# Kernel optimization log

Hardware: AMD Instinct MI355X
Metric: run time of the kernel (lower is better)

The kernel has to match this reference:

```python
import math
import jax, jax.numpy as jnp
import numpy as np

HEADS = 8
LOG_APPROX_VAR = math.log(0.01)  # self.var = 0.01, non-trainable


def clustering(x, approx_log_var, mu, log_var, log_prior):
    """Faithful port of DisentangledAttention.clustering (mi_estimation=False).
    x: [B,H,L,D]; approx_log_var: [B,H,L]; mu/log_var: [H,C,D]; log_prior: [H,C].
    Returns (cluster_probs [B,H,L,C], kl_loss [B,1,1], div_loss [B])."""
    B, H, L, D = x.shape
    xe = x[:, :, :, None, :]                      # [B,H,L,1,D]
    mue = mu[:, None, :, :]                       # [H,1,C,D]
    alv = approx_log_var[:, :, :, None, None]     # [B,H,L,1,1]
    avar = jnp.exp(alv)
    lv = log_var[:, None, :, :]                   # [H,1,C,D]
    var = jnp.exp(lv)
    logp = jax.nn.log_softmax(log_prior, axis=-1)  # [H,C]

    mse = (xe - mue) ** 2 / var                   # [B,H,L,C,D]
    log_pdf = -0.5 * mse.sum(-1) - D * math.pi - 0.5 * lv.sum(-1)  # [B,H,L,C]
    log_pdf = log_pdf + logp[:, None, :]
    log_probs = jax.nn.log_softmax(log_pdf, axis=-1)
    probs = jnp.exp(log_probs)                    # [B,H,L,C]

    logp_b = logp[None, :, None, :]               # broadcast prior log-probs
    prior = jnp.exp(logp_b)
    # F.kl_div(log_probs, prior) = prior * (log(prior) - log_probs)
    kl = (prior * (logp_b - log_probs)).sum(-1).mean(axis=(1, 2))            # [B]
    kl = kl + 0.5 * (probs * (mse + avar / var + lv).sum(-1)).sum(-1).mean(axis=(1, 2))
    kl = kl - 0.5 * jnp.mean(((1.0 + alv).sum(-1)) * D, axis=(1, 2, 3))
    kl_loss = kl.reshape(-1, 1, 1)

    eyeL = jnp.eye(L, dtype=x.dtype)
    div = jnp.einsum('bhqc,bhkc->bhqk', probs, probs)   # [B,H,L,L]
    div = (div - eyeL) ** 2
    wmask = eyeL * 1.25 + (1.0 - eyeL) * 0.75
    div_loss = (div * wmask).mean(axis=(1, 2, 3))       # [B]
    return probs, kl_loss, div_loss


def setup_inputs() -> dict:
    k = jax.random.key(0)
    ks = jax.random.split(k, 10)
    B, L, D, H, C = 4, 1024, 512, HEADS, 8
    Dk = D // H
    lin_std = 1.0 / math.sqrt(2.0 * D)  # xavier_normal gain=1/sqrt(2)
    return {
        'query': jax.random.normal(ks[0], (B, L, D), jnp.float32),
        'key': jax.random.normal(ks[1], (B, L, D), jnp.float32),
        'value': jax.random.normal(ks[2], (B, L, D), jnp.float32),
        'padding_mask': jnp.zeros((B, 1, L), jnp.float32),
        'Wq': jax.random.normal(ks[3], (D, D), jnp.float32) * lin_std,
        'bq': jnp.zeros((D,), jnp.float32),
        'Wk': jax.random.normal(ks[4], (D, D), jnp.float32) * lin_std,
        'bk': jnp.zeros((D,), jnp.float32),
        'Wv': jax.random.normal(ks[5], (D, D), jnp.float32) * lin_std,
        'bv': jnp.zeros((D,), jnp.float32),
        'Wo': jax.random.normal(ks[6], (D, D), jnp.float32) * lin_std,
        'bo': jnp.zeros((D,), jnp.float32),
        'tok_mu': jax.random.normal(ks[7], (H, C, Dk), jnp.float32) * 0.1,
        'tok_log_var': jnp.zeros((H, C, Dk), jnp.float32),
        'tok_log_prior': jnp.full((H, C), math.log(1.0 / C), jnp.float32),
    }


def reference(query, key, value, padding_mask, Wq, bq, Wk, bk, Wv, bv, Wo, bo,
              tok_mu, tok_log_var, tok_log_prior):
    B, L, D = query.shape
    H = HEADS
    Dk = D // H

    # GMM clustering on raw (unprojected) per-head query/key, eval mode (no reparam noise)
    qh = query.reshape(B, L, H, Dk).transpose(0, 2, 1, 3)  # [B,H,L,Dk]
    kh = key.reshape(B, L, H, Dk).transpose(0, 2, 1, 3)
    alv = jnp.full((B, H, L), LOG_APPROX_VAR, dtype=query.dtype)
    probs_q, kl_q, div_q = clustering(qh, alv, tok_mu, tok_log_var, tok_log_prior)
    probs_k, kl_k, div_k = clustering(kh, alv, tok_mu, tok_log_var, tok_log_prior)

    # Disentangled mask: tokens sharing clusters attend (mask==1 means blocked)
    sim = jnp.einsum('bhqc,bhkc->bhqk', probs_q, probs_k)   # [B,H,L,L]
    cmask = jnp.clip(1.0 - sim + padding_mask[:, :, None, :], 0.0, 1.0)

    # Projections + scaled softmax attention (per softmax_attention/full_attention)
    q = (query @ Wq.T + bq).reshape(B, L, H, Dk).transpose(0, 2, 1, 3) / math.sqrt(Dk)
    kk = (key @ Wk.T + bk).reshape(B, L, H, Dk).transpose(0, 2, 1, 3)
    v = (value @ Wv.T + bv).reshape(B, L, H, Dk).transpose(0, 2, 1, 3)
    scores = jnp.einsum('bhqd,bhkd->bhqk', q, kk) + jax.lax.stop_gradient(cmask) * (-10000.0)
    attn = jax.nn.softmax(scores, axis=-1) * (1.0 - cmask)
    out = jnp.einsum('bhqk,bhkd->bhqd', attn, v).transpose(0, 2, 1, 3).reshape(B, L, D)
    out = out @ Wo.T + bo

    kl_loss = kl_q + kl_k                      # [B,1,1]
    div_loss = (div_q + div_k).reshape(-1, 1, 1)  # [B,1,1]
    return out, kl_loss, div_loss
```

## Files before the change

### kernel.cpp

```cpp
#include <hip/hip_runtime.h>
#include <hip/hip_bf16.h>
#include <math.h>

#define NB 4
#define NL 1024
#define ND 512
#define NH 8
#define NC 8
#define NDK 64

static constexpr float KL3_CONST = 115.36544595161891f;

typedef __bf16 bf16x8 __attribute__((ext_vector_type(8)));
typedef float  f32x4v __attribute__((ext_vector_type(4)));
typedef unsigned short u16x4 __attribute__((ext_vector_type(4)));
typedef unsigned short u16x8 __attribute__((ext_vector_type(8)));

__device__ __forceinline__ unsigned short bf16u(float f) {
    return __builtin_bit_cast(unsigned short, (__bf16)f);
}

struct GemmArgs {
    const void* A; const float* W; const float* bias; void* out;
    float scale; int abf; int obf; int brow; int ostr; int vmap;
};

__device__ __forceinline__ void gemm_body(const GemmArgs& g, unsigned char* smem)
{
    unsigned short* As = (unsigned short*)smem;
    unsigned short* Ws = (unsigned short*)(smem + 5120);
    const int tid = threadIdx.x;
    int n0, m0;
    if (g.vmap) {
        const int linear = blockIdx.y * 4 + blockIdx.x;
        n0 = (linear & 31) * 128;
        m0 = (linear >> 5) * 64;
    } else {
        n0 = blockIdx.x * 128;
        m0 = blockIdx.y * 64;
    }

    const int w = tid >> 6, lane = tid & 63;
    const int r16 = lane & 15, quad = lane >> 4;
    const int arow = tid >> 2, akc = tid & 3;
    const int wrow = tid >> 1, wkc = tid & 1;

    f32x4v acc[8];
#pragma unroll
    for (int n = 0; n < 8; ++n) acc[n] = (f32x4v){0.f, 0.f, 0.f, 0.f};

    auto ldA = [&](int k0) -> u16x8 {
        if (g.abf) {
            return *(const u16x8*)((const unsigned short*)g.A + (size_t)(m0 + arow) * 512 + k0 + akc * 8);
        }
        const float* ap = (const float*)g.A + (size_t)(m0 + arow) * 512 + k0 + akc * 8;
        const float4 a0 = *(const float4*)ap, a1 = *(const float4*)(ap + 4);
        return (u16x8){ bf16u(a0.x), bf16u(a0.y), bf16u(a0.z), bf16u(a0.w),
                        bf16u(a1.x), bf16u(a1.y), bf16u(a1.z), bf16u(a1.w) };
    };
    auto ldW = [&](int k0, u16x8* dst) {
        const float* wp = (const float*)g.W + (size_t)(n0 + wrow) * 512 + k0 + wkc * 16;
        const float4 w0 = *(const float4*)wp,       w1 = *(const float4*)(wp + 4);
        const float4 w2 = *(const float4*)(wp + 8), w3 = *(const float4*)(wp + 12);
        dst[0] = (u16x8){ bf16u(w0.x), bf16u(w0.y), bf16u(w0.z), bf16u(w0.w),
                          bf16u(w1.x), bf16u(w1.y), bf16u(w1.z), bf16u(w1.w) };
        dst[1] = (u16x8){ bf16u(w2.x), bf16u(w2.y), bf16u(w2.z), bf16u(w2.w),
                          bf16u(w3.x), bf16u(w3.y), bf16u(w3.z), bf16u(w3.w) };
    };
    auto store_stage = [&](const u16x8& sa, const u16x8* sw) {
        *(u16x8*)(As + arow * 40 + akc * 8) = sa;
        *(u16x8*)(Ws + wrow * 40 + wkc * 16) = sw[0];
        *(u16x8*)(Ws + wrow * 40 + wkc * 16 + 8) = sw[1];
    };
    auto mfma_half = [&]() {
        bf16x8 af = *(const bf16x8*)(As + (w * 16 + r16) * 40 + quad * 8);
#pragma unroll
        for (int ni = 0; ni < 8; ++ni) {
            bf16x8 bfr = *(const bf16x8*)(Ws + (ni * 16 + r16) * 40 + quad * 8);
            acc[ni] = __builtin_amdgcn_mfma_f32_16x16x32_bf16(af, bfr, acc[ni], 0, 0, 0);
        }
    };

    u16x8 sa0 = ldA(0),  sw0[2]; ldW(0, sw0);
    u16x8 sa1 = ldA(32), sw1[2]; ldW(32, sw1);

    for (int k0 = 0; k0 < 512; k0 += 64) {
        __syncthreads();
        store_stage(sa0, sw0);
        __syncthreads();
        if (k0 + 64 < 512) { sa0 = ldA(k0 + 64); ldW(k0 + 64, sw0); }
        mfma_half();

        __syncthreads();
        store_stage(sa1, sw1);
        __syncthreads();
        if (k0 + 96 < 512) { sa1 = ldA(k0 + 96); ldW(k0 + 96, sw1); }
        mfma_half();
    }

#pragma unroll
    for (int ni = 0; ni < 8; ++ni) {
        const int col = n0 + ni * 16 + r16;
        const float bcol = g.brow ? 0.f : g.bias[col];
#pragma unroll
        for (int i = 0; i < 4; ++i) {
            const int row = m0 + w * 16 + quad * 4 + i;
            const float bv = g.brow ? g.bias[row] : bcol;
            const float v = (acc[ni][i] + bv) * g.scale;
            if (g.obf) ((unsigned short*)g.out)[(size_t)row * g.ostr + col] = bf16u(v);
            else       ((float*)g.out)[(size_t)row * g.ostr + col] = v;
        }
    }
}

__device__ __forceinline__ void cluster_body(
    const float* __restrict__ query, const float* __restrict__ key,
    const float* __restrict__ tok_mu, const float* __restrict__ tok_log_var,
    const float* __restrict__ tok_log_prior,
    float* __restrict__ probs_q, float* __restrict__ probs_k,
    float* __restrict__ klp, float* __restrict__ divp, float* __restrict__ Gp,
    int linear, unsigned char* smem)
{
    float* mu_s    = (float*)smem;
    float* iv_s    = (float*)(smem + 2048);
    float* Pl      = (float*)(smem + 4096);
    float* Gpart   = (float*)(smem + 13312);
    float* red_s   = (float*)(smem + 14336);
    float* lvsum_s = (float*)(smem + 14368);
    float* alpha_s = (float*)(smem + 14400);
    float* logp_s  = (float*)(smem + 14432);
    float* prior_s = (float*)(smem + 14464);

    const int tid  = threadIdx.x;
    const int side = linear >> 7;
    const int rem  = linear & 127;
    const int bh   = rem >> 2, chunk = rem & 3;
    const int b    = bh >> 3, h = bh & 7;
    const int blocklin = side * 128 + bh * 4 + chunk;
    const float* src = side ? key : query;
    float* probs_out = side ? probs_k : probs_q;

    for (int i = tid; i < 512; i += 256) {
        mu_s[i] = tok_mu[h * 512 + i];
        float lv = tok_log_var[h * 512 + i];
        iv_s[i] = __expf(-lv);
    }
    if (tid < 8) {
        float ls = 0.f, al = 0.f;
        for (int d = 0; d < 64; ++d) {
            float lv = tok_log_var[(h * 8 + tid) * 64 + d];
            ls += lv;
            al += 0.01f * __expf(-lv) + lv;
        }
        lvsum_s[tid] = ls; alpha_s[tid] = al;
    }
    if (tid == 0) {
        float lp[8]; float mx = -1e30f;
        for (int c = 0; c < 8; ++c) { lp[c] = tok_log_prior[h * 8 + c]; mx = fmaxf(mx, lp[c]); }
        float se = 0.f;
        for (int c = 0; c < 8; ++c) se += __expf(lp[c] - mx);
        float lse = mx + __logf(se);
        for (int c = 0; c < 8; ++c) { logp_s[c] = lp[c] - lse; prior_s[c] = __expf(lp[c] - lse); }
    }
    __syncthreads();

    const int l = chunk * 256 + tid;
    const float4* xp = (const float4*)(src + ((size_t)(b * NL + l)) * ND + h * NDK);
    float4 xr[16];
#pragma unroll
    for (int i = 0; i < 16; ++i) xr[i] = xp[i];

    float ms[8];
#pragma unroll
    for (int c = 0; c < 8; ++c) {
        const float4* mc = (const float4*)(mu_s + c * 64);
        const float4* ic = (const float4*)(iv_s + c * 64);
        float s = 0.f;
#pragma unroll
        for (int i = 0; i < 16; ++i) {
            float4 m4 = mc[i], v4 = ic[i], x4 = xr[i];
            float dx = x4.x - m4.x; s = fmaf(dx * dx, v4.x, s);
            float dy = x4.y - m4.y; s = fmaf(dy * dy, v4.y, s);
            float dz = x4.z - m4.z; s = fmaf(dz * dz, v4.z, s);
            float dw = x4.w - m4.w; s = fmaf(dw * dw, v4.w, s);
        }
        ms[c] = s;
    }

    float lpdf[8]; float mx = -1e30f;
#pragma unroll
    for (int c = 0; c < 8; ++c) {
        lpdf[c] = -0.5f * (ms[c] + lvsum_s[c]) + logp_s[c];
        mx = fmaxf(mx, lpdf[c]);
    }
    float e[8]; float se = 0.f;
#pragma unroll
    for (int c = 0; c < 8; ++c) { e[c] = __expf(lpdf[c] - mx); se += e[c]; }
    float lse = __logf(se);
    float inv = 1.f / se;
    float p[8]; float kl1 = 0.f, kl2 = 0.f, sqq = 0.f;
#pragma unroll
    for (int c = 0; c < 8; ++c) {
        p[c] = e[c] * inv;
        float logprob = lpdf[c] - mx - lse;
        kl1 += prior_s[c] * (logp_s[c] - logprob);
        kl2 += p[c] * (ms[c] + alpha_s[c]);
        sqq = fmaf(p[c], p[c], sqq);
    }

    float* po = probs_out + ((size_t)((b * NH + h) * NL + l)) * NC;
    ((float4*)po)[0] = make_float4(p[0], p[1], p[2], p[3]);
    ((float4*)po)[1] = make_float4(p[4], p[5], p[6], p[7]);
#pragma unroll
    for (int c = 0; c < 8; ++c) Pl[tid * 9 + c] = p[c];

    float dterm = 1.25f * (sqq - 1.f) * (sqq - 1.f) - 0.75f * sqq * sqq;
    float klv = kl1 + 0.5f * kl2;
    __syncthreads();

    {
        int qt = tid >> 6, pos = tid & 63, c1 = pos >> 3, c2 = pos & 7;
        float g = 0.f;
        for (int i = 0; i < 64; ++i) {
            int ll = qt * 64 + i;
            g = fmaf(Pl[ll * 9 + c1], Pl[ll * 9 + c2], g);
        }
        Gpart[qt * 64 + pos] = g;
    }

#pragma unroll
    for (int o = 32; o > 0; o >>= 1) {
        klv   += __shfl_down(klv, o);
        dterm += __shfl_down(dterm, o);
    }
    if ((tid & 63) == 0) { red_s[tid >> 6] = klv; red_s[4 + (tid >> 6)] = dterm; }
    __syncthreads();
    if (tid == 0) {
        klp[blocklin]  = red_s[0] + red_s[1] + red_s[2] + red_s[3];
        divp[blocklin] = red_s[4] + red_s[5] + red_s[6] + red_s[7];
    }
    if (tid < 64)
        Gp[(size_t)blocklin * 64 + tid] =
            Gpart[tid] + Gpart[64 + tid] + Gpart[128 + tid] + Gpart[192 + tid];
}

__global__ __launch_bounds__(256) void fused_front(
    GemmArgs g0, GemmArgs g1, GemmArgs g2,
    const float* query, const float* key,
    const float* tok_mu, const float* tok_log_var, const float* tok_log_prior,
    float* probs_q, float* probs_k,
    float* klp, float* divp, float* Gp)
{
    __shared__ alignas(16) unsigned char smem[15488];
    if (blockIdx.z == 3) {
        const int linear = blockIdx.y * 4 + blockIdx.x;
        cluster_body(query, key, tok_mu, tok_log_var, tok_log_prior,
                     probs_q, probs_k, klp, divp, Gp, linear, smem);
        return;
    }
    GemmArgs g = (blockIdx.z == 0) ? g0 : ((blockIdx.z == 1) ? g1 : g2);
    gemm_body(g, smem);
}

#define APAD 72

__global__ __launch_bounds__(128) void attn_mfma3s_kernel(
    const unsigned short* __restrict__ qp16, const unsigned short* __restrict__ kp16,
    const unsigned short* __restrict__ vtp16,
    const float* __restrict__ probs_q, const float* __restrict__ probs_k,
    const float* __restrict__ padding_mask,
    float* __restrict__ pO, float* __restrict__ pML)
{
    const int tid = threadIdx.x, lane = tid & 63, w = tid >> 6;
    const int r16 = lane & 15, quad = lane >> 4;
    const int b = blockIdx.z >> 1, s = blockIdx.z & 1;
    const int h = blockIdx.y;
    const int qt = blockIdx.x;
    const int qbase = qt * 32;
    const int sb = ((b * 8 + h) << 5) | qt;

    __shared__ alignas(16) unsigned short Ks[64 * APAD];
    __shared__ alignas(16) unsigned short Vt[64 * APAD];
    __shared__ alignas(16) unsigned short Ps[2][16 * APAD];
    __shared__ float pk_s[8 * 65];
    __shared__ float pm_s[64];

    bf16x8 qa[2];
    {
        const unsigned short* qrow = qp16 + ((size_t)(b * NL + qbase + w * 16 + r16)) * ND + h * NDK;
        qa[0] = *(const bf16x8*)(qrow + quad * 8);
        qa[1] = *(const bf16x8*)(qrow + 32 + quad * 8);
    }
    float pq[4][8];
#pragma unroll
    for (int i = 0; i < 4; ++i) {
        const float* pr = probs_q + ((size_t)((b * NH + h) * NL + qbase + w * 16 + quad * 4 + i)) * NC;
        float4 a = ((const float4*)pr)[0], c = ((const float4*)pr)[1];
        pq[i][0] = a.x; pq[i][1] = a.y; pq[i][2] = a.z; pq[i][3] = a.w;
        pq[i][4] = c.x; pq[i][5] = c.y; pq[i][6] = c.z; pq[i][7] = c.w;
    }

    f32x4v oacc[4];
#pragma unroll
    for (int n = 0; n < 4; ++n) oacc[n] = (f32x4v){0.f, 0.f, 0.f, 0.f};
    float m_i[4] = {-1e30f, -1e30f, -1e30f, -1e30f};
    float l_i[4] = {0.f, 0.f, 0.f, 0.f};

    for (int kt = 0; kt < 8; ++kt) {
        const int key0 = s * 512 + kt * 64;
        __syncthreads();

#pragma unroll
        for (int i = 0; i < 4; ++i) {
            const int c = i * 128 + tid;
            const int row = c >> 3, c8 = c & 7;
            u16x8 kv = *(const u16x8*)(kp16 + ((size_t)(b * NL + key0 + row)) * ND + h * NDK + c8 * 8);
            *(u16x8*)(Ks + row * APAD + c8 * 8) = kv;
            u16x8 vv = *(const u16x8*)(vtp16 + ((size_t)(h * 64 + row)) * (NB * NL) + b * NL + key0 + c8 * 8);
            *(u16x8*)(Vt + row * APAD + c8 * 8) = vv;
        }
        {
            const int key = tid >> 1, half = tid & 1;
            float4 p = *(const float4*)(probs_k + ((size_t)((b * NH + h) * NL + key0 + key)) * NC + half * 4);
            pk_s[(half * 4 + 0) * 65 + key] = p.x;
            pk_s[(half * 4 + 1) * 65 + key] = p.y;
            pk_s[(half * 4 + 2) * 65 + key] = p.z;
            pk_s[(half * 4 + 3) * 65 + key] = p.w;
        }
        if (tid < 64) pm_s[tid] = padding_mask[b * NL + key0 + tid];
        __syncthreads();

        f32x4v sacc[4];
#pragma unroll
        for (int t = 0; t < 4; ++t) {
            sacc[t] = (f32x4v){0.f, 0.f, 0.f, 0.f};
            bf16x8 kb0 = *(const bf16x8*)(Ks + (t * 16 + r16) * APAD + quad * 8);
            bf16x8 kb1 = *(const bf16x8*)(Ks + (t * 16 + r16) * APAD + 32 + quad * 8);
            sacc[t] = __builtin_amdgcn_mfma_f32_16x16x32_bf16(qa[0], kb0, sacc[t], 0, 0, 0);
            sacc[t] = __builtin_amdgcn_mfma_f32_16x16x32_bf16(qa[1], kb1, sacc[t], 0, 0, 0);
        }

        float sc[4][4], wgt[4][4];
#pragma unroll
        for (int t = 0; t < 4; ++t) {
            const int keyl = t * 16 + r16;
            float pkc[8];
#pragma unroll
            for (int c = 0; c < 8; ++c) pkc[c] = pk_s[c * 65 + keyl];
            const float pmv = pm_s[keyl];
#pragma unroll
            for (int i = 0; i < 4; ++i) {
                float sim = 0.f;
#pragma unroll
                for (int c = 0; c < 8; ++c) sim = fmaf(pq[i][c], pkc[c], sim);
                float cm = 1.f - sim + pmv;
                cm = fminf(fmaxf(cm, 0.f), 1.f);
                sc[t][i] = sacc[t][i] - 10000.f * cm;
                wgt[t][i] = 1.f - cm;
            }
        }

        float mx[4];
#pragma unroll
        for (int i = 0; i < 4; ++i)
            mx[i] = fmaxf(fmaxf(sc[0][i], sc[1][i]), fmaxf(sc[2][i], sc[3][i]));
#pragma unroll
        for (int o = 1; o < 16; o <<= 1) {
#pragma unroll
            for (int i = 0; i < 4; ++i) mx[i] = fmaxf(mx[i], __shfl_xor(mx[i], o));
        }
        float rr[4];
#pragma unroll
        for (int i = 0; i < 4; ++i) {
            const float mnew = fmaxf(m_i[i], mx[i]);
            rr[i] = __expf(m_i[i] - mnew);
            m_i[i] = mnew;
            l_i[i] *= rr[i];
        }
#pragma unroll
        for (int n = 0; n < 4; ++n) {
            oacc[n][0] *= rr[0]; oacc[n][1] *= rr[1];
            oacc[n][2] *= rr[2]; oacc[n][3] *= rr[3];
        }
        float lad[4] = {0.f, 0.f, 0.f, 0.f};
#pragma unroll
        for (int t = 0; t < 4; ++t) {
#pragma unroll
            for (int i = 0; i < 4; ++i) {
                const float p = __expf(sc[t][i] - m_i[i]);
                lad[i] += p;
                Ps[w][(quad * 4 + i) * APAD + t * 16 + r16] = bf16u(p * wgt[t][i]);
            }
        }
#pragma unroll
        for (int o = 1; o < 16; o <<= 1) {
#pragma unroll
            for (int i = 0; i < 4; ++i) lad[i] += __shfl_xor(lad[i], o);
        }
#pragma unroll
        for (int i = 0; i < 4; ++i) l_i[i] += lad[i];

        bf16x8 pa0 = *(const bf16x8*)(Ps[w] + r16 * APAD + quad * 8);
        bf16x8 pa1 = *(const bf16x8*)(Ps[w] + r16 * APAD + 32 + quad * 8);
#pragma unroll
        for (int n = 0; n < 4; ++n) {
            bf16x8 vb0 = *(const bf16x8*)(Vt + (n * 16 + r16) * APAD + quad * 8);
            bf16x8 vb1 = *(const bf16x8*)(Vt + (n * 16 + r16) * APAD + 32 + quad * 8);
            oacc[n] = __builtin_amdgcn_mfma_f32_16x16x32_bf16(pa0, vb0, oacc[n], 0, 0, 0);
            oacc[n] = __builtin_amdgcn_mfma_f32_16x16x32_bf16(pa1, vb1, oacc[n], 0, 0, 0);
        }
    }

    float* po = pO + ((size_t)sb * 2 + s) * 2048;
#pragma unroll
    for (int i = 0; i < 4; ++i) {
        const int row = w * 16 + quad * 4 + i;
#pragma unroll
        for (int n = 0; n < 4; ++n)
            po[row * 64 + n * 16 + r16] = oacc[n][i];
    }
    if (r16 == 0) {
        float* pml = pML + ((size_t)sb * 2 + s) * 64;
#pragma unroll
        for (int i = 0; i < 4; ++i) {
            const int row = w * 16 + quad * 4 + i;
            pml[row * 2]     = m_i[i];
            pml[row * 2 + 1] = l_i[i];
        }
    }
}

__device__ __forceinline__ void finalize_body(
    const float* __restrict__ klp, const float* __restrict__ divp,
    const float* __restrict__ Gp, float* __restrict__ out_tail)
{
    const int tid = threadIdx.x, b = tid >> 6, lane = tid & 63;
    float gsum = 0.f;
#pragma unroll
    for (int s = 0; s < 2; ++s)
#pragma unroll
        for (int h = 0; h < 8; ++h) {
            const int base = s * 128 + (b * 8 + h) * 4;
            float Ge = 0.f;
#pragma unroll
            for (int x = 0; x < 4; ++x) Ge += Gp[(size_t)(base + x) * 64 + lane];
            gsum = fmaf(Ge, Ge, gsum);
        }
    const int s = lane >> 5, rem = lane & 31, h = rem >> 2, x = rem & 3;
    const int idx = s * 128 + (b * 8 + h) * 4 + x;
    float klv = klp[idx];
    float dvv = divp[idx];
#pragma unroll
    for (int o = 32; o > 0; o >>= 1) {
        gsum += __shfl_down(gsum, o);
        klv  += __shfl_down(klv, o);
        dvv  += __shfl_down(dvv, o);
    }
    if (lane == 0) {
        out_tail[b]     = klv * (1.0f / 8192.0f) + 2.0f * KL3_CONST;
        out_tail[4 + b] = (dvv + 0.75f * gsum) * (1.0f / 8388608.0f);
    }
}

__global__ __launch_bounds__(256) void merge_fin_kernel(
    const float* __restrict__ pO, const float* __restrict__ pML,
    unsigned short* __restrict__ ao16,
    const float* __restrict__ klp, const float* __restrict__ divp,
    const float* __restrict__ Gp, float* __restrict__ out_tail)
{
    if (blockIdx.x == 1024) { finalize_body(klp, divp, Gp, out_tail); return; }
    const int gid = blockIdx.x * 256 + threadIdx.x;
    const int sb = gid >> 8, rem = gid & 255;
    const int row = rem >> 3, d0 = (rem & 7) * 8;

    const float2 ml0 = *(const float2*)(pML + ((size_t)sb * 2 + 0) * 64 + row * 2);
    const float2 ml1 = *(const float2*)(pML + ((size_t)sb * 2 + 1) * 64 + row * 2);
    const float M = fmaxf(ml0.x, ml1.x);
    const float e0 = __expf(ml0.x - M), e1 = __expf(ml1.x - M);
    const float inv = 1.f / fmaf(ml0.y, e0, ml1.y * e1);
    const float f0 = e0 * inv, f1 = e1 * inv;

    const float* p0 = pO + ((size_t)sb * 2 + 0) * 2048 + row * 64 + d0;
    const float* p1 = pO + ((size_t)sb * 2 + 1) * 2048 + row * 64 + d0;
    const int qt = sb & 31, bh = sb >> 5, h = bh & 7, b = bh >> 3;
    unsigned short* orow = ao16 + ((size_t)(b * NL + qt * 32 + row)) * ND + h * NDK + d0;

    const float4 a0 = *(const float4*)p0,       a1 = *(const float4*)(p0 + 4);
    const float4 c0 = *(const float4*)p1,       c1 = *(const float4*)(p1 + 4);
    u16x8 ov = { bf16u(a0.x * f0 + c0.x * f1), bf16u(a0.y * f0 + c0.y * f1),
                 bf16u(a0.z * f0 + c0.z * f1), bf16u(a0.w * f0 + c0.w * f1),
                 bf16u(a1.x * f0 + c1.x * f1), bf16u(a1.y * f0 + c1.y * f1),
                 bf16u(a1.z * f0 + c1.z * f1), bf16u(a1.w * f0 + c1.w * f1) };
    *(u16x8*)orow = ov;
}

__global__ __launch_bounds__(256) void gemm_single(GemmArgs g)
{
    __shared__ alignas(16) unsigned char smem[15488];
    gemm_body(g, smem);
}

extern "C" void kernel_launch(void* const* d_in, const int* in_sizes, int n_in,
                              void* d_out, int out_size, void* d_ws, size_t ws_size,
                              hipStream_t stream)
{
    const float* query        = (const float*)d_in[0];
    const float* key          = (const float*)d_in[1];
    const float* value        = (const float*)d_in[2];
    const float* padding_mask = (const float*)d_in[3];
    const float* Wq = (const float*)d_in[4];
    const float* bq = (const float*)d_in[5];
    const float* Wk = (const float*)d_in[6];
    const float* bk = (const float*)d_in[7];
    const float* Wv = (const float*)d_in[8];
    const float* bv = (const float*)d_in[9];
    const float* Wo = (const float*)d_in[10];
    const float* bo = (const float*)d_in[11];
    const float* tok_mu        = (const float*)d_in[12];
    const float* tok_log_var   = (const float*)d_in[13];
    const float* tok_log_prior = (const float*)d_in[14];

    float* ws = (float*)d_ws;
    const size_t FS = 1048576;
    unsigned short* qp16  = (unsigned short*)ws;
    unsigned short* kp16  = (unsigned short*)(ws + FS);
    unsigned short* vtp16 = (unsigned short*)(ws + 2 * FS);
    unsigned short* ao16  = (unsigned short*)(ws + 3 * FS);
    float* probs_q = ws + 4 * FS;
    float* probs_k = probs_q + (size_t)NB * NH * NL * NC;
    float* pO      = probs_k + (size_t)NB * NH * NL * NC;
    float* pML     = pO + 4194304;
    float* klp     = pML + 131072;
    float* divp    = klp + 256;
    float* Gp      = divp + 256;

    GemmArgs gq {query, Wq, bq, qp16, 0.125f, 0, 1, 0, 512, 0};
    GemmArgs gk {key,   Wk, bk, kp16, 1.f,    0, 1, 0, 512, 0};
    GemmArgs gvt{Wv, value, bv, vtp16, 1.f,   0, 1, 1, 4096, 1};
    fused_front<<<dim3(4, 64, 4), 256, 0, stream>>>(
        gq, gk, gvt, query, key, tok_mu, tok_log_var, tok_log_prior,
        probs_q, probs_k, klp, divp, Gp);

    attn_mfma3s_kernel<<<dim3(32, NH, NB * 2), 128, 0, stream>>>(
        qp16, kp16, vtp16, probs_q, probs_k, padding_mask, pO, pML);

    merge_fin_kernel<<<1025, 256, 0, stream>>>(
        pO, pML, ao16, klp, divp, Gp, (float*)d_out + (size_t)NB * NL * ND);

    GemmArgs go{ao16, Wo, bo, d_out, 1.f, 1, 0, 0, 512, 0};
    gemm_single<<<dim3(4, 64, 1), 256, 0, stream>>>(go);
}
```

Baseline: 209.6 us.

## Load K/V tiles directly from global into registers, dropping LDS staging and barriers

The attention kernel no longer stages K, V^T, probs_k and padding mask tiles through shared memory with two __syncthreads per key tile. Each wave now reads its MFMA operands straight from global memory (relying on L1/L2 since both waves share the same keys). This removes the barriers and LDS round-trips and lowers LDS use, which may raise occupancy. The cost is duplicated global loads across the two waves and less coalesced, higher-latency operand fetches right before the MFMAs.

Measured after the change: 242.2 us. 1.16x slower.

```diff
diff --git a/kernel.cpp b/kernel.cpp
--- a/kernel.cpp
+++ b/kernel.cpp
@@ -264,7 +264,7 @@
 
 #define APAD 72
 
-__global__ __launch_bounds__(128) void attn_mfma3s_kernel(
+__global__ __launch_bounds__(128) void attn_mfma4_kernel(
     const unsigned short* __restrict__ qp16, const unsigned short* __restrict__ kp16,
     const unsigned short* __restrict__ vtp16,
     const float* __restrict__ probs_q, const float* __restrict__ probs_k,
@@ -279,11 +279,7 @@
     const int qbase = qt * 32;
     const int sb = ((b * 8 + h) << 5) | qt;
 
-    __shared__ alignas(16) unsigned short Ks[64 * APAD];
-    __shared__ alignas(16) unsigned short Vt[64 * APAD];
     __shared__ alignas(16) unsigned short Ps[2][16 * APAD];
-    __shared__ float pk_s[8 * 65];
-    __shared__ float pm_s[64];
 
     bf16x8 qa[2];
     {
@@ -300,6 +296,11 @@
         pq[i][4] = c.x; pq[i][5] = c.y; pq[i][6] = c.z; pq[i][7] = c.w;
     }
 
+    const unsigned short* kbase = kp16 + ((size_t)(b * NL + s * 512)) * ND + h * NDK;
+    const unsigned short* vbase = vtp16 + ((size_t)(h * 64)) * (NB * NL) + b * NL + s * 512;
+    const float* pkbase = probs_k + ((size_t)((b * NH + h) * NL + s * 512)) * NC;
+    const float* pmbase = padding_mask + b * NL + s * 512;
+
     f32x4v oacc[4];
 #pragma unroll
     for (int n = 0; n < 4; ++n) oacc[n] = (f32x4v){0.f, 0.f, 0.f, 0.f};
@@ -307,53 +308,35 @@
     float l_i[4] = {0.f, 0.f, 0.f, 0.f};
 
     for (int kt = 0; kt < 8; ++kt) {
-        const int key0 = s * 512 + kt * 64;
-        __syncthreads();
-
-#pragma unroll
-        for (int i = 0; i < 4; ++i) {
-            const int c = i * 128 + tid;
-            const int row = c >> 3, c8 = c & 7;
-            u16x8 kv = *(const u16x8*)(kp16 + ((size_t)(b * NL + key0 + row)) * ND + h * NDK + c8 * 8);
-            *(u16x8*)(Ks + row * APAD + c8 * 8) = kv;
-            u16x8 vv = *(const u16x8*)(vtp16 + ((size_t)(h * 64 + row)) * (NB * NL) + b * NL + key0 + c8 * 8);
-            *(u16x8*)(Vt + row * APAD + c8 * 8) = vv;
-        }
-        {
-            const int key = tid >> 1, half = tid & 1;
-            float4 p = *(const float4*)(probs_k + ((size_t)((b * NH + h) * NL + key0 + key)) * NC + half * 4);
-            pk_s[(half * 4 + 0) * 65 + key] = p.x;
-            pk_s[(half * 4 + 1) * 65 + key] = p.y;
-            pk_s[(half * 4 + 2) * 65 + key] = p.z;
-            pk_s[(half * 4 + 3) * 65 + key] = p.w;
-        }
-        if (tid < 64) pm_s[tid] = padding_mask[b * NL + key0 + tid];
-        __syncthreads();
+        const int k0 = kt * 64;
 
         f32x4v sacc[4];
+        float pkc[4][8], pmv[4];
 #pragma unroll
         for (int t = 0; t < 4; ++t) {
+            const int keyl = k0 + t * 16 + r16;
+            const unsigned short* krow = kbase + (size_t)keyl * ND;
+            bf16x8 kb0 = *(const bf16x8*)(krow + quad * 8);
+            bf16x8 kb1 = *(const bf16x8*)(krow + 32 + quad * 8);
             sacc[t] = (f32x4v){0.f, 0.f, 0.f, 0.f};
-            bf16x8 kb0 = *(const bf16x8*)(Ks + (t * 16 + r16) * APAD + quad * 8);
-            bf16x8 kb1 = *(const bf16x8*)(Ks + (t * 16 + r16) * APAD + 32 + quad * 8);
             sacc[t] = __builtin_amdgcn_mfma_f32_16x16x32_bf16(qa[0], kb0, sacc[t], 0, 0, 0);
             sacc[t] = __builtin_amdgcn_mfma_f32_16x16x32_bf16(qa[1], kb1, sacc[t], 0, 0, 0);
+            const float* pr = pkbase + (size_t)keyl * NC;
+            float4 pa_ = ((const float4*)pr)[0], pb_ = ((const float4*)pr)[1];
+            pkc[t][0] = pa_.x; pkc[t][1] = pa_.y; pkc[t][2] = pa_.z; pkc[t][3] = pa_.w;
+            pkc[t][4] = pb_.x; pkc[t][5] = pb_.y; pkc[t][6] = pb_.z; pkc[t][7] = pb_.w;
+            pmv[t] = pmbase[keyl];
         }
 
         float sc[4][4], wgt[4][4];
 #pragma unroll
         for (int t = 0; t < 4; ++t) {
-            const int keyl = t * 16 + r16;
-            float pkc[8];
-#pragma unroll
-            for (int c = 0; c < 8; ++c) pkc[c] = pk_s[c * 65 + keyl];
-            const float pmv = pm_s[keyl];
 #pragma unroll
             for (int i = 0; i < 4; ++i) {
                 float sim = 0.f;
 #pragma unroll
-                for (int c = 0; c < 8; ++c) sim = fmaf(pq[i][c], pkc[c], sim);
-                float cm = 1.f - sim + pmv;
+                for (int c = 0; c < 8; ++c) sim = fmaf(pq[i][c], pkc[t][c], sim);
+                float cm = 1.f - sim + pmv[t];
                 cm = fminf(fmaxf(cm, 0.f), 1.f);
                 sc[t][i] = sacc[t][i] - 10000.f * cm;
                 wgt[t][i] = 1.f - cm;
@@ -404,8 +387,9 @@
         bf16x8 pa1 = *(const bf16x8*)(Ps[w] + r16 * APAD + 32 + quad * 8);
 #pragma unroll
         for (int n = 0; n < 4; ++n) {
-            bf16x8 vb0 = *(const bf16x8*)(Vt + (n * 16 + r16) * APAD + quad * 8);
-            bf16x8 vb1 = *(const bf16x8*)(Vt + (n * 16 + r16) * APAD + 32 + quad * 8);
+            const unsigned short* vrow = vbase + (size_t)(n * 16 + r16) * (NB * NL) + k0;
+            bf16x8 vb0 = *(const bf16x8*)(vrow + quad * 8);
+            bf16x8 vb1 = *(const bf16x8*)(vrow + 32 + quad * 8);
             oacc[n] = __builtin_amdgcn_mfma_f32_16x16x32_bf16(pa0, vb0, oacc[n], 0, 0, 0);
             oacc[n] = __builtin_amdgcn_mfma_f32_16x16x32_bf16(pa1, vb1, oacc[n], 0, 0, 0);
         }
@@ -541,7 +525,7 @@
         gq, gk, gvt, query, key, tok_mu, tok_log_var, tok_log_prior,
         probs_q, probs_k, klp, divp, Gp);
 
-    attn_mfma3s_kernel<<<dim3(32, NH, NB * 2), 128, 0, stream>>>(
+    attn_mfma4_kernel<<<dim3(32, NH, NB * 2), 128, 0, stream>>>(
         qp16, kp16, vtp16, probs_q, probs_k, padding_mask, pO, pML);
 
     merge_fin_kernel<<<1025, 256, 0, stream>>>(
```

## Enlarge attention block to 64 queries and register-prefetch next K/V tile

Applied to the files above, without the earlier changes.

The attention kernel now runs 256 threads (4 waves) per block covering 64 query rows, so each K/V/probs_k tile loaded into shared memory is reused by twice as many waves. Global loads for tile kt+2 are issued into registers while tile kt is computed, then stored to shared memory after a barrier, hiding global latency behind MFMA work. The grid halves and the output indexing is remapped to keep the same partial-output layout for the merge kernel. The trade-off is extra registers for the staged tile and fewer blocks in flight.

After: 197.3 us. 5.9% less time.

```diff
diff --git a/kernel.cpp b/kernel.cpp
--- a/kernel.cpp
+++ b/kernel.cpp
@@ -264,7 +264,7 @@
 
 #define APAD 72
 
-__global__ __launch_bounds__(128) void attn_mfma3s_kernel(
+__global__ __launch_bounds__(256) void attn_mfma5_kernel(
     const unsigned short* __restrict__ qp16, const unsigned short* __restrict__ kp16,
     const unsigned short* __restrict__ vtp16,
     const float* __restrict__ probs_q, const float* __restrict__ probs_k,
@@ -276,14 +276,17 @@
     const int b = blockIdx.z >> 1, s = blockIdx.z & 1;
     const int h = blockIdx.y;
     const int qt = blockIdx.x;
-    const int qbase = qt * 32;
-    const int sb = ((b * 8 + h) << 5) | qt;
+    const int qbase = qt * 64;
 
     __shared__ alignas(16) unsigned short Ks[64 * APAD];
     __shared__ alignas(16) unsigned short Vt[64 * APAD];
-    __shared__ alignas(16) unsigned short Ps[2][16 * APAD];
+    __shared__ alignas(16) unsigned short Ps[4][16 * APAD];
     __shared__ float pk_s[8 * 65];
     __shared__ float pm_s[64];
+
+    const int c0row = tid >> 3,        c0c8 = tid & 7;
+    const int c1row = (tid + 256) >> 3, c1c8 = tid & 7;
+    const int pkey = tid >> 1, phalf = tid & 1;
 
     bf16x8 qa[2];
     {
@@ -306,28 +309,40 @@
     float m_i[4] = {-1e30f, -1e30f, -1e30f, -1e30f};
     float l_i[4] = {0.f, 0.f, 0.f, 0.f};
 
+    u16x8 rk0, rk1, rv0, rv1;
+    float4 rpk;
+    float rpm;
+
+    auto stage_load = [&](int kt) {
+        const int key0 = s * 512 + kt * 64;
+        rk0 = *(const u16x8*)(kp16 + ((size_t)(b * NL + key0 + c0row)) * ND + h * NDK + c0c8 * 8);
+        rk1 = *(const u16x8*)(kp16 + ((size_t)(b * NL + key0 + c1row)) * ND + h * NDK + c1c8 * 8);
+        rv0 = *(const u16x8*)(vtp16 + ((size_t)(h * 64 + c0row)) * (NB * NL) + b * NL + key0 + c0c8 * 8);
+        rv1 = *(const u16x8*)(vtp16 + ((size_t)(h * 64 + c1row)) * (NB * NL) + b * NL + key0 + c1c8 * 8);
+        if (tid < 128)
+            rpk = *(const float4*)(probs_k + ((size_t)((b * NH + h) * NL + key0 + pkey)) * NC + phalf * 4);
+        if (tid < 64)
+            rpm = padding_mask[b * NL + key0 + tid];
+    };
+    auto stage_store = [&]() {
+        *(u16x8*)(Ks + c0row * APAD + c0c8 * 8) = rk0;
+        *(u16x8*)(Ks + c1row * APAD + c1c8 * 8) = rk1;
+        *(u16x8*)(Vt + c0row * APAD + c0c8 * 8) = rv0;
+        *(u16x8*)(Vt + c1row * APAD + c1c8 * 8) = rv1;
+        if (tid < 128) {
+            pk_s[(phalf * 4 + 0) * 65 + pkey] = rpk.x;
+            pk_s[(phalf * 4 + 1) * 65 + pkey] = rpk.y;
+            pk_s[(phalf * 4 + 2) * 65 + pkey] = rpk.z;
+            pk_s[(phalf * 4 + 3) * 65 + pkey] = rpk.w;
+        }
+        if (tid < 64) pm_s[tid] = rpm;
+    };
+
+    stage_load(0);
+    stage_store();
+    stage_load(1);
+
     for (int kt = 0; kt < 8; ++kt) {
-        const int key0 = s * 512 + kt * 64;
-        __syncthreads();
-
-#pragma unroll
-        for (int i = 0; i < 4; ++i) {
-            const int c = i * 128 + tid;
-            const int row = c >> 3, c8 = c & 7;
-            u16x8 kv = *(const u16x8*)(kp16 + ((size_t)(b * NL + key0 + row)) * ND + h * NDK + c8 * 8);
-            *(u16x8*)(Ks + row * APAD + c8 * 8) = kv;
-            u16x8 vv = *(const u16x8*)(vtp16 + ((size_t)(h * 64 + row)) * (NB * NL) + b * NL + key0 + c8 * 8);
-            *(u16x8*)(Vt + row * APAD + c8 * 8) = vv;
-        }
-        {
-            const int key = tid >> 1, half = tid & 1;
-            float4 p = *(const float4*)(probs_k + ((size_t)((b * NH + h) * NL + key0 + key)) * NC + half * 4);
-            pk_s[(half * 4 + 0) * 65 + key] = p.x;
-            pk_s[(half * 4 + 1) * 65 + key] = p.y;
-            pk_s[(half * 4 + 2) * 65 + key] = p.z;
-            pk_s[(half * 4 + 3) * 65 + key] = p.w;
-        }
-        if (tid < 64) pm_s[tid] = padding_mask[b * NL + key0 + tid];
         __syncthreads();
 
         f32x4v sacc[4];
@@ -409,21 +424,28 @@
             oacc[n] = __builtin_amdgcn_mfma_f32_16x16x32_bf16(pa0, vb0, oacc[n], 0, 0, 0);
             oacc[n] = __builtin_amdgcn_mfma_f32_16x16x32_bf16(pa1, vb1, oacc[n], 0, 0, 0);
         }
-    }
-
-    float* po = pO + ((size_t)sb * 2 + s) * 2048;
+
+        __syncthreads();
+        if (kt < 7) {
+            stage_store();
+            if (kt < 6) stage_load(kt + 2);
+        }
+    }
+
+    const int sb32 = (((b * 8 + h) << 5) | (qt * 2 + (w >> 1)));
+    float* po = pO + ((size_t)sb32 * 2 + s) * 2048;
 #pragma unroll
     for (int i = 0; i < 4; ++i) {
-        const int row = w * 16 + quad * 4 + i;
+        const int row = (w & 1) * 16 + quad * 4 + i;
 #pragma unroll
         for (int n = 0; n < 4; ++n)
             po[row * 64 + n * 16 + r16] = oacc[n][i];
     }
     if (r16 == 0) {
-        float* pml = pML + ((size_t)sb * 2 + s) * 64;
+        float* pml = pML + ((size_t)sb32 * 2 + s) * 64;
 #pragma unroll
         for (int i = 0; i < 4; ++i) {
-            const int row = w * 16 + quad * 4 + i;
+            const int row = (w & 1) * 16 + quad * 4 + i;
             pml[row * 2]     = m_i[i];
             pml[row * 2 + 1] = l_i[i];
         }
@@ -541,7 +563,7 @@
         gq, gk, gvt, query, key, tok_mu, tok_log_var, tok_log_prior,
         probs_q, probs_k, klp, divp, Gp);
 
-    attn_mfma3s_kernel<<<dim3(32, NH, NB * 2), 128, 0, stream>>>(
+    attn_mfma5_kernel<<<dim3(16, NH, NB * 2), 256, 0, stream>>>(
         qp16, kp16, vtp16, probs_q, probs_k, padding_mask, pO, pML);
 
     merge_fin_kernel<<<1025, 256, 0, stream>>>(
```
